# Performance work log

Hardware: AMD Instinct MI355X
Metric: run time of the kernel (lower is better)

## Reference

```python
import jax, jax.numpy as jnp
import numpy as np

B, L, H, N, NL = 2, 160000, 128, 64, 4
TS, MR, CLS, LMAX = 1001, 16, 88, 1024
REP = TS * MR  # 16016


def setup_inputs() -> dict:
    key = jax.random.key(0)
    ks = jax.random.split(key, 16)
    def g(k, shape, s=0.02):
        return jax.random.normal(k, shape, jnp.float32) * s
    return {
        "x": jax.random.normal(ks[0], (B, L), jnp.float32),
        "enc_w": g(ks[1], (1, H), 1.0),
        "enc_b": g(ks[2], (H,)),
        "log_dt": jax.random.uniform(ks[3], (NL, H), jnp.float32, float(np.log(1e-3)), float(np.log(1e-1))),
        "log_A_real": jnp.log(0.5 * jnp.ones((NL, H, N), jnp.float32)),
        "A_imag": jnp.tile((np.pi * np.arange(N, dtype=np.float32))[None, None, :], (NL, H, 1)),
        "C_re": g(ks[4], (NL, H, N), 0.5 ** 0.5),
        "C_im": g(ks[5], (NL, H, N), 0.5 ** 0.5),
        "D": g(ks[6], (NL, H), 1.0),
        "out_w": g(ks[7], (NL, 2 * H, H), H ** -0.5),
        "out_b": g(ks[8], (NL, 2 * H)),
        "ln_g": jnp.ones((NL, H), jnp.float32),
        "ln_b": jnp.zeros((NL, H), jnp.float32),
        "dec_w": g(ks[9], (H, REP), H ** -0.5),
        "dec_b": g(ks[10], (REP,)),
        "head_w": g(ks[11], (4, MR, CLS), MR ** -0.5),
        "head_b": g(ks[12], (4, CLS)),
    }


def _s4_layer(u, log_dt, log_A_real, A_imag, C_re, C_im, D, out_w, out_b):
    # u: (B, H, L). S4D-style diagonal SSM kernel of length LMAX + FFT causal conv.
    dt = jnp.exp(log_dt)                         # (H,)
    A = -jnp.exp(log_A_real) + 1j * A_imag       # (H, N)
    C = C_re + 1j * C_im                         # (H, N)
    dtA = A * dt[:, None]                        # (H, N)
    Ct = C * (jnp.exp(dtA) - 1.0) / A            # ZOH-ish discretization
    l = jnp.arange(LMAX)
    vand = jnp.exp(dtA[:, :, None] * l)          # (H, N, LMAX) Vandermonde
    K = 2.0 * jnp.real(jnp.einsum('hn,hnl->hl', Ct, vand))  # (H, LMAX)
    n = L + LMAX                                 # linear (causal) conv via FFT
    uf = jnp.fft.rfft(u, n=n)                    # (B, H, n//2+1)
    kf = jnp.fft.rfft(K, n=n)                    # (H, n//2+1)
    y = jnp.fft.irfft(uf * kf[None], n=n)[..., :L]
    y = y + D[None, :, None] * u                 # skip connection
    y = jax.nn.gelu(y)
    # position-wise output linear H -> 2H, then GLU
    z = jnp.einsum('bhl,ph->bpl', y, out_w) + out_b[None, :, None]
    a, b = jnp.split(z, 2, axis=1)
    return a * jax.nn.sigmoid(b)


def _layernorm(v, g, b):
    # v: (B, L, H), normalize over H
    mu = v.mean(-1, keepdims=True)
    var = v.var(-1, keepdims=True)
    return (v - mu) / jnp.sqrt(var + 1e-5) * g + b


def reference(x, enc_w, enc_b, log_dt, log_A_real, A_imag, C_re, C_im, D,
              out_w, out_b, ln_g, ln_b, dec_w, dec_b, head_w, head_b):
    # encoder: (B, L, 1) -> (B, L, H)
    h = x[..., None] * enc_w[0][None, None, :] + enc_b  # (B, L, H)
    u = jnp.swapaxes(h, 1, 2)                            # (B, H, L)
    for i in range(NL):
        z = _s4_layer(u, log_dt[i], log_A_real[i], A_imag[i], C_re[i], C_im[i],
                      D[i], out_w[i], out_b[i])
        u = z + u                                        # residual
        v = _layernorm(jnp.swapaxes(u, 1, 2), ln_g[i], ln_b[i])  # post-norm
        u = jnp.swapaxes(v, 1, 2)
    feat = jnp.swapaxes(u, 1, 2).mean(axis=1)            # (B, H) mean-pool over L
    rep = feat @ dec_w + dec_b                           # (B, REP)
    rep = rep.reshape(B, TS, MR)                         # (B, 1001, 16)
    # 4 heads: [reg_onset, reg_offset, frame, velocity] stacked -> (4, B, TS, CLS)
    outs = jnp.einsum('btm,kmc->kbtc', rep, head_w) + head_b[:, None, None, :]
    return outs
```

## Files before the change

kernel.cpp:

```cpp
#include <hip/hip_runtime.h>
#include <math.h>

#define B_ 2
#define L_ 160000
#define H_ 128
#define N_ 64
#define NL_ 4
#define LMAX_ 1024
#define TS_ 1001
#define MR_ 16
#define CLS_ 88
#define REP_ 16016

#define NSUB_ 79
#define NJ_ 40
#define WIN_ 3208
#define WINS_ 3216
#define OUTB_ 2048
#define KE_STRIDE_ 1536

typedef unsigned short ushort_t;
typedef unsigned int uint_t;
typedef short bf16x8 __attribute__((ext_vector_type(8)));
typedef float f32x4 __attribute__((ext_vector_type(4)));

__device__ __forceinline__ float bf2f(ushort_t h) {
  uint_t u = ((uint_t)h) << 16;
  return __uint_as_float(u);
}
__device__ __forceinline__ ushort_t f2bf(float f) {
  uint_t u = __float_as_uint(f);
  uint_t r = (u + 0x7fffu + ((u >> 16) & 1u)) >> 16;
  return (ushort_t)r;
}

__global__ __launch_bounds__(256) void k_encode(const float* __restrict__ x,
                                                const float* __restrict__ enc_w,
                                                const float* __restrict__ enc_b,
                                                ushort_t* __restrict__ u) {
  int idx = blockIdx.x * 256 + threadIdx.x;
  int idx8 = idx * 8;
  int b = idx8 / (H_ * L_);
  int rem = idx8 - b * (H_ * L_);
  int h = rem / L_;
  int l = rem - h * L_;
  float w = enc_w[h], bb = enc_b[h];
  float4 x0 = *(const float4*)(x + b * L_ + l);
  float4 x1 = *(const float4*)(x + b * L_ + l + 4);
  union { ushort_t s[8]; uint4 v; } o;
  o.s[0] = f2bf(x0.x * w + bb); o.s[1] = f2bf(x0.y * w + bb);
  o.s[2] = f2bf(x0.z * w + bb); o.s[3] = f2bf(x0.w * w + bb);
  o.s[4] = f2bf(x1.x * w + bb); o.s[5] = f2bf(x1.y * w + bb);
  o.s[6] = f2bf(x1.z * w + bb); o.s[7] = f2bf(x1.w * w + bb);
  *(uint4*)(u + (size_t)(b * H_ + h) * L_ + l) = o.v;
}

__global__ __launch_bounds__(256) void k_ct(const float* __restrict__ log_dt,
                                            const float* __restrict__ log_A_real,
                                            const float* __restrict__ A_imag,
                                            const float* __restrict__ C_re,
                                            const float* __restrict__ C_im,
                                            float* __restrict__ ct,
                                            float* __restrict__ feat) {
  int idx = blockIdx.x * 256 + threadIdx.x;
  if (idx < B_ * H_) feat[idx] = 0.f;
  if (idx >= NL_ * H_ * N_) return;
  int h = (idx / N_) % H_;
  int i = idx / (N_ * H_);
  float dt = expf(log_dt[i * H_ + h]);
  float are = -expf(log_A_real[idx]);
  float aim = A_imag[idx];
  float dr = are * dt, di = aim * dt;
  float e = expf(dr);
  float si, co;
  sincosf(di, &si, &co);
  float er = e * co - 1.0f;
  float ei = e * si;
  float den = are * are + aim * aim;
  float qr = (er * are + ei * aim) / den;
  float qi = (ei * are - er * aim) / den;
  float cr = C_re[idx], cim = C_im[idx];
  double dd = (double)aim * (double)dt * 0.15915494309189535;
  dd -= floor(dd);
  uint_t P = (uint_t)(unsigned long long)(dd * 4294967296.0);
  ct[idx * 4 + 0] = dr;
  ct[idx * 4 + 1] = __uint_as_float(P);
  ct[idx * 4 + 2] = cr * qr - cim * qi;
  ct[idx * 4 + 3] = cr * qi + cim * qr;
}

__global__ __launch_bounds__(256) void k_ke(const float* __restrict__ ct,
                                            ushort_t* __restrict__ Ke) {
  int q = blockIdx.x & 3;
  int ih = blockIdx.x >> 2;
  __shared__ float4 cs[N_];
  if (threadIdx.x < N_) cs[threadIdx.x] = ((const float4*)ct)[ih * N_ + threadIdx.x];
  __syncthreads();
  for (int s = q * 384 + threadIdx.x; s < (q + 1) * 384; s += 256) {
    int d = s - 256;
    float val = 0.f;
    if (d >= 0 && d < LMAX_) {
      float fl = (float)d;
      float acc = 0.f;
      #pragma unroll 4
      for (int n = 0; n < N_; n++) {
        float4 qv = cs[n];
        float e = __expf(qv.x * fl);
        uint_t ph = __float_as_uint(qv.y) * (uint_t)d;
        float ang = (float)ph * 2.3283064365386963e-10f;
        float si = __builtin_amdgcn_sinf(ang);
        float co = __builtin_amdgcn_cosf(ang);
        acc += e * (qv.z * co - qv.w * si);
      }
      val = 2.f * acc;
    }
    Ke[(size_t)ih * KE_STRIDE_ + s] = f2bf(val);
  }
}

__global__ __launch_bounds__(256) void k_wprep(const float* __restrict__ W,
                                               ushort_t* __restrict__ Wb) {
  int idx = blockIdx.x * 256 + threadIdx.x;
  Wb[idx] = f2bf(W[idx]);
}

__global__ __launch_bounds__(256) void k_conv_mfma(const ushort_t* __restrict__ u,
                                                   const ushort_t* __restrict__ Ke,
                                                   const float* __restrict__ Dv,
                                                   ushort_t* __restrict__ y,
                                                   int layer) {
  int sub = blockIdx.x % NSUB_;
  int bh = blockIdx.x / NSUB_;
  int h = bh & (H_ - 1);
  int O0 = sub * OUTB_;
  int Gmax = O0 + 2063;
  __shared__ ushort_t win[4 * WINS_];
  __shared__ ushort_t kes[KE_STRIDE_];
  int tid = threadIdx.x;
  int lane = tid & 63, w = tid >> 6;
  int m = lane & 15, g = lane >> 4;

  {
    const ushort_t* keh0 = Ke + (size_t)(layer * H_ + h) * KE_STRIDE_;
    if (tid < KE_STRIDE_ / 8)
      *(bf16x8*)(kes + 8 * tid) = *(const bf16x8*)(keh0 + 8 * tid);
  }

  const ushort_t* ubh = u + (size_t)bh * L_;
  for (int T = tid; T < WIN_ / 8; T += 256) {
    int topt = Gmax - 8 * T;
    ushort_t vb[16];
    if (topt - 15 >= 0 && topt < L_) {
      union { uint4 q[2]; ushort_t s[16]; } ld;
      ld.q[0] = *(const uint4*)(ubh + topt - 15);
      ld.q[1] = *(const uint4*)(ubh + topt - 7);
      #pragma unroll
      for (int d = 0; d < 16; d++) vb[d] = ld.s[15 - d];
    } else {
      #pragma unroll
      for (int d = 0; d < 16; d++) {
        int gl = topt - d;
        vb[d] = (gl >= 0 && gl < L_) ? ubh[gl] : (ushort_t)0;
      }
    }
    #pragma unroll
    for (int p = 0; p < 4; p++) {
      union { bf16x8 v; ushort_t s[8]; } gr;
      #pragma unroll
      for (int e = 0; e < 8; e++) gr.s[e] = vb[p + e];
      *(bf16x8*)((char*)win + p * (2 * WINS_) + 16 * T) = gr.v;
    }
  }
  __syncthreads();

  const char* wb = (const char*)win;
  const ushort_t* kf0 = kes + 16 * m + 8 * g;
  int l0A = O0 + (w << 9);
  f32x4 accA = {0.f, 0.f, 0.f, 0.f}, accB = {0.f, 0.f, 0.f, 0.f};
  int t0 = Gmax - l0A - m + 8 * g - 256;
  bf16x8 ring[8];
  #pragma unroll
  for (int s = -8; s < NJ_; s++) {
    int tS = t0 + (s << 5);
    int pS = tS & 3;
    const char* base = wb + pS * (2 * WINS_) + 2 * (tS - pS);
    union { bf16x8 v; short4 h[2]; } f;
    f.h[0] = *(const short4*)base;
    f.h[1] = *(const short4*)(base + 8);
    if (s >= 0)
      accA = __builtin_amdgcn_mfma_f32_16x16x32_bf16(f.v, ring[s & 7], accA, 0, 0, 0);
    if (s <= 31) {
      bf16x8 kn = *(const bf16x8*)(kf0 + 32 * (s + 8));
      accB = __builtin_amdgcn_mfma_f32_16x16x32_bf16(f.v, kn, accB, 0, 0, 0);
      ring[(s + 8) & 7] = kn;
    }
  }

  float Dh = Dv[layer * H_ + h];
  ushort_t* ybh = y + (size_t)bh * L_;
  #pragma unroll
  for (int tile = 0; tile < 2; tile++) {
    f32x4 acc = tile ? accB : accA;
    int l0 = l0A + tile * 256;
    int outb = l0 + 16 * m + 4 * g;
    int tu = Gmax - outb - 3;
    int pu = tu & 3;
    union { short4 s4; ushort_t us[4]; } uu;
    uu.s4 = *(const short4*)(wb + pu * (2 * WINS_) + 2 * (tu - pu));
    union { ushort_t s[4]; short4 v; } pk;
    #pragma unroll
    for (int r = 0; r < 4; r++) {
      float uval = bf2f(uu.us[3 - r]);
      float v = acc[r] + Dh * uval;
      float z2 = 1.5957691216057308f * (v + 0.044715f * v * v * v);
      pk.s[r] = f2bf(v / (1.f + __expf(-z2)));
    }
    if (outb < L_) *(short4*)(ybh + outb) = pk.v;
  }
}

__global__ __launch_bounds__(256) void k_fused(const ushort_t* __restrict__ y,
                                               const ushort_t* __restrict__ Wb,
                                               const float* __restrict__ ob,
                                               ushort_t* __restrict__ u,
                                               const float* __restrict__ lng,
                                               const float* __restrict__ lnb,
                                               int last,
                                               float* __restrict__ feat) {
  __shared__ ushort_t yT[64 * 136];
  __shared__ float redS[4 * 64] __attribute__((aligned(16)));
  __shared__ float redQ[4 * 64] __attribute__((aligned(16)));
  __shared__ float redM[64] __attribute__((aligned(16)));
  __shared__ float redR[64] __attribute__((aligned(16)));
  int lblk = blockIdx.x, b = blockIdx.y;
  int lc0 = lblk * 64;
  int tid = threadIdx.x;
  int lane = tid & 63, w = tid >> 6;
  int m = lane & 15, g = lane >> 4;

  bf16x8 Wf[4][4];
  #pragma unroll
  for (int pj = 0; pj < 4; pj++) {
    int pbase = (pj < 2) ? (32 * w + 16 * pj) : (128 + 32 * w + 16 * (pj - 2));
    const ushort_t* wrow = Wb + (pbase + m) * 128 + 8 * g;
    #pragma unroll
    for (int ks = 0; ks < 4; ks++)
      Wf[pj][ks] = *(const bf16x8*)(wrow + 32 * ks);
  }

  short4 uoh[2][4];
  float oba[2], obs[2], gam[2], bet[2];
  #pragma unroll
  for (int pj = 0; pj < 2; pj++) {
    int pa = 32 * w + 16 * pj + m;
    const ushort_t* urow = u + (size_t)(b * H_ + pa) * L_ + lc0;
    #pragma unroll
    for (int lj = 0; lj < 4; lj++)
      uoh[pj][lj] = *(const short4*)(urow + 16 * lj + 4 * g);
    oba[pj] = ob[pa];
    obs[pj] = ob[pa + 128];
    gam[pj] = lng[pa];
    bet[pj] = lnb[pa];
  }

  {
    int s = tid & 7;
    int kkb = tid >> 3;
    #pragma unroll
    for (int p = 0; p < 4; p++) {
      int kk = kkb + 32 * p;
      const ushort_t* yp = y + ((size_t)b * H_ + kk) * L_ + lc0 + 8 * s;
      uint4 vv = *(const uint4*)yp;
      const ushort_t* hp = (const ushort_t*)&vv;
      int sw = 8 * ((kk >> 3) ^ s) + (kk & 7);
      #pragma unroll
      for (int e = 0; e < 8; e++)
        yT[(8 * s + e) * 136 + sw] = hp[e];
    }
  }
  __syncthreads();

  f32x4 acc[4][4];
  #pragma unroll
  for (int pj = 0; pj < 4; pj++)
    #pragma unroll
    for (int lj = 0; lj < 4; lj++) acc[pj][lj] = (f32x4){0.f, 0.f, 0.f, 0.f};
  #pragma unroll
  for (int ks = 0; ks < 4; ks++) {
    bf16x8 yf[4];
    #pragma unroll
    for (int lj = 0; lj < 4; lj++) {
      int l = 16 * lj + m;
      yf[lj] = *(const bf16x8*)(yT + l * 136 + 8 * ((4 * ks + g) ^ (l >> 3)));
    }
    #pragma unroll
    for (int pj = 0; pj < 4; pj++)
      #pragma unroll
      for (int lj = 0; lj < 4; lj++)
        acc[pj][lj] = __builtin_amdgcn_mfma_f32_16x16x32_bf16(yf[lj], Wf[pj][ks],
                                                              acc[pj][lj], 0, 0, 0);
  }

  #pragma unroll
  for (int pj = 0; pj < 2; pj++) {
    #pragma unroll
    for (int lj = 0; lj < 4; lj++) {
      #pragma unroll
      for (int r = 0; r < 4; r++) {
        float a = acc[pj][lj][r] + oba[pj];
        float sv = acc[pj + 2][lj][r] + obs[pj];
        float uor = bf2f(((const ushort_t*)&uoh[pj][lj])[r]);
        acc[pj][lj][r] = a * (1.f / (1.f + __expf(-sv))) + uor;
      }
    }
  }

  #pragma unroll
  for (int lj = 0; lj < 4; lj++) {
    #pragma unroll
    for (int r = 0; r < 4; r++) {
      float v0 = acc[0][lj][r], v1 = acc[1][lj][r];
      float s = v0 + v1, q = v0 * v0 + v1 * v1;
      s += __shfl_xor(s, 1);  q += __shfl_xor(q, 1);
      s += __shfl_xor(s, 2);  q += __shfl_xor(q, 2);
      s += __shfl_xor(s, 4);  q += __shfl_xor(q, 4);
      s += __shfl_xor(s, 8);  q += __shfl_xor(q, 8);
      if (m == 0) {
        int l = 16 * lj + 4 * g + r;
        redS[w * 64 + l] = s;
        redQ[w * 64 + l] = q;
      }
    }
  }
  __syncthreads();
  if (tid < 64) {
    float s = redS[tid] + redS[64 + tid] + redS[128 + tid] + redS[192 + tid];
    float q = redQ[tid] + redQ[64 + tid] + redQ[128 + tid] + redQ[192 + tid];
    float mean = s * (1.f / 128.f);
    float var = q * (1.f / 128.f) - mean * mean;
    redM[tid] = mean;
    redR[tid] = rsqrtf(var + 1e-5f);
  }
  __syncthreads();

  #pragma unroll
  for (int pj = 0; pj < 2; pj++) {
    int pa = 32 * w + 16 * pj + m;
    ushort_t* urow = u + (size_t)(b * H_ + pa) * L_ + lc0;
    float pool = 0.f;
    #pragma unroll
    for (int lj = 0; lj < 4; lj++) {
      int l0 = 16 * lj + 4 * g;
      f32x4 mn = *(const f32x4*)(redM + l0);
      f32x4 rs = *(const f32x4*)(redR + l0);
      if (!last) {
        union { ushort_t s[4]; short4 v; } pk;
        #pragma unroll
        for (int r = 0; r < 4; r++)
          pk.s[r] = f2bf((acc[pj][lj][r] - mn[r]) * rs[r] * gam[pj] + bet[pj]);
        *(short4*)(urow + l0) = pk.v;
      } else {
        #pragma unroll
        for (int r = 0; r < 4; r++)
          pool += (acc[pj][lj][r] - mn[r]) * rs[r] * gam[pj] + bet[pj];
      }
    }
    if (last) {
      pool += __shfl_xor(pool, 16);
      pool += __shfl_xor(pool, 32);
      if (g == 0) atomicAdd(&feat[b * H_ + pa], pool * (1.f / L_));
    }
  }
}

__global__ __launch_bounds__(256) void k_dec(const float* __restrict__ feat,
                                             const float* __restrict__ dw,
                                             const float* __restrict__ db,
                                             float* __restrict__ rep) {
  int idx = blockIdx.x * 256 + threadIdx.x;
  if (idx >= B_ * REP_) return;
  int b = idx / REP_, r = idx - b * REP_;
  float s = db[r];
  #pragma unroll 8
  for (int h = 0; h < H_; h++) s = fmaf(feat[b * H_ + h], dw[h * REP_ + r], s);
  rep[idx] = s;
}

__global__ __launch_bounds__(256) void k_head(const float* __restrict__ rep,
                                              const float* __restrict__ hw,
                                              const float* __restrict__ hb,
                                              float* __restrict__ out) {
  int idx = blockIdx.x * 256 + threadIdx.x;
  if (idx >= 4 * B_ * TS_ * CLS_) return;
  int c = idx % CLS_;
  int t = (idx / CLS_) % TS_;
  int b = (idx / (CLS_ * TS_)) % B_;
  int k = idx / (CLS_ * TS_ * B_);
  float s = hb[k * CLS_ + c];
  const float* rp = rep + ((long long)b * TS_ + t) * MR_;
  #pragma unroll
  for (int m = 0; m < MR_; m++) s = fmaf(rp[m], hw[(k * MR_ + m) * CLS_ + c], s);
  out[idx] = s;
}

extern "C" void kernel_launch(void* const* d_in, const int* in_sizes, int n_in,
                              void* d_out, int out_size, void* d_ws, size_t ws_size,
                              hipStream_t stream) {
  const float* x = (const float*)d_in[0];
  const float* enc_w = (const float*)d_in[1];
  const float* enc_b = (const float*)d_in[2];
  const float* log_dt = (const float*)d_in[3];
  const float* log_A_real = (const float*)d_in[4];
  const float* A_imag = (const float*)d_in[5];
  const float* C_re = (const float*)d_in[6];
  const float* C_im = (const float*)d_in[7];
  const float* Dv = (const float*)d_in[8];
  const float* out_w = (const float*)d_in[9];
  const float* out_b = (const float*)d_in[10];
  const float* ln_g = (const float*)d_in[11];
  const float* ln_b = (const float*)d_in[12];
  const float* dec_w = (const float*)d_in[13];
  const float* dec_b = (const float*)d_in[14];
  const float* head_w = (const float*)d_in[15];
  const float* head_b = (const float*)d_in[16];

  if (ws_size < 167000000ULL) return;

  float* ws = (float*)d_ws;
  ushort_t* u = (ushort_t*)ws;
  ushort_t* y = (ushort_t*)(ws + 20480000);
  ushort_t* Ke = (ushort_t*)(ws + 20480000 + 20480000);
  float* ct = ws + 20480000 + 20480000 + 393216;
  ushort_t* Wb = (ushort_t*)(ct + 131072);
  float* feat = ct + 131072 + 65536;
  float* rep = feat + 256;

  k_encode<<<(B_ * H_ * L_ / 8 + 255) / 256, 256, 0, stream>>>(x, enc_w, enc_b, u);
  k_ct<<<(NL_ * H_ * N_ + 255) / 256, 256, 0, stream>>>(log_dt, log_A_real, A_imag,
                                                        C_re, C_im, ct, feat);
  k_ke<<<NL_ * H_ * 4, 256, 0, stream>>>(ct, Ke);
  k_wprep<<<NL_ * 256 * 128 / 256, 256, 0, stream>>>(out_w, Wb);

  for (int i = 0; i < NL_; i++) {
    k_conv_mfma<<<B_ * H_ * NSUB_, 256, 0, stream>>>(u, Ke, Dv, y, i);
    k_fused<<<dim3(L_ / 64, B_), 256, 0, stream>>>(
        y, Wb + (size_t)i * 256 * 128, out_b + i * 256, u,
        ln_g + i * H_, ln_b + i * H_, (i == NL_ - 1) ? 1 : 0, feat);
  }
  k_dec<<<(B_ * REP_ + 255) / 256, 256, 0, stream>>>(feat, dec_w, dec_b, rep);
  k_head<<<(4 * B_ * TS_ * CLS_ + 255) / 256, 256, 0, stream>>>(rep, head_w, head_b,
                                                               (float*)d_out);
}
```

Before: 929.7 us.

## Process four L-tiles per block in k_fused with register prefetch of next tile

The fused projection/GLU/LayerNorm kernel now walks four consecutive 64-column tiles per block instead of one. The weight fragments and per-channel constants are loaded once and reused across the four tiles. The next tile's y and residual u values are prefetched into registers while the current tile's MFMAs and reductions run. The grid shrinks by a factor of four. In exchange, register pressure rises from the extra prefetch buffers, which may lower occupancy, and there are fewer blocks to spread across the CUs.

```diff
diff --git a/kernel.cpp b/kernel.cpp
--- a/kernel.cpp
+++ b/kernel.cpp
@@ -233,10 +233,11 @@
   __shared__ float redM[64] __attribute__((aligned(16)));
   __shared__ float redR[64] __attribute__((aligned(16)));
   int lblk = blockIdx.x, b = blockIdx.y;
-  int lc0 = lblk * 64;
   int tid = threadIdx.x;
   int lane = tid & 63, w = tid >> 6;
   int m = lane & 15, g = lane >> 4;
+  int s = tid & 7, kkb = tid >> 3;
+  int Lbase = lblk * 256;
 
   bf16x8 Wf[4][4];
   #pragma unroll
@@ -247,125 +248,163 @@
     for (int ks = 0; ks < 4; ks++)
       Wf[pj][ks] = *(const bf16x8*)(wrow + 32 * ks);
   }
-
-  short4 uoh[2][4];
   float oba[2], obs[2], gam[2], bet[2];
   #pragma unroll
   for (int pj = 0; pj < 2; pj++) {
     int pa = 32 * w + 16 * pj + m;
-    const ushort_t* urow = u + (size_t)(b * H_ + pa) * L_ + lc0;
-    #pragma unroll
-    for (int lj = 0; lj < 4; lj++)
-      uoh[pj][lj] = *(const short4*)(urow + 16 * lj + 4 * g);
     oba[pj] = ob[pa];
     obs[pj] = ob[pa + 128];
     gam[pj] = lng[pa];
     bet[pj] = lnb[pa];
   }
 
-  {
-    int s = tid & 7;
-    int kkb = tid >> 3;
+  uint4 sr[4];
+  short4 un[2][4];
+  #pragma unroll
+  for (int p = 0; p < 4; p++)
+    sr[p] = *(const uint4*)(y + ((size_t)b * H_ + kkb + 32 * p) * L_ + Lbase + 8 * s);
+  #pragma unroll
+  for (int pj = 0; pj < 2; pj++) {
+    int pa = 32 * w + 16 * pj + m;
+    const ushort_t* urow = u + (size_t)(b * H_ + pa) * L_ + Lbase;
+    #pragma unroll
+    for (int lj = 0; lj < 4; lj++)
+      un[pj][lj] = *(const short4*)(urow + 16 * lj + 4 * g);
+  }
+
+  float poolAcc[2] = {0.f, 0.f};
+
+  #pragma unroll
+  for (int st = 0; st < 4; st++) {
+    int lc0 = Lbase + st * 64;
+
     #pragma unroll
     for (int p = 0; p < 4; p++) {
       int kk = kkb + 32 * p;
-      const ushort_t* yp = y + ((size_t)b * H_ + kk) * L_ + lc0 + 8 * s;
-      uint4 vv = *(const uint4*)yp;
-      const ushort_t* hp = (const ushort_t*)&vv;
+      const ushort_t* hp = (const ushort_t*)&sr[p];
       int sw = 8 * ((kk >> 3) ^ s) + (kk & 7);
       #pragma unroll
       for (int e = 0; e < 8; e++)
         yT[(8 * s + e) * 136 + sw] = hp[e];
     }
-  }
-  __syncthreads();
-
-  f32x4 acc[4][4];
-  #pragma unroll
-  for (int pj = 0; pj < 4; pj++)
-    #pragma unroll
-    for (int lj = 0; lj < 4; lj++) acc[pj][lj] = (f32x4){0.f, 0.f, 0.f, 0.f};
-  #pragma unroll
-  for (int ks = 0; ks < 4; ks++) {
-    bf16x8 yf[4];
+    __syncthreads();
+
+    uint4 srn[4];
+    short4 unn[2][4];
+    if (st < 3) {
+      int lc1 = lc0 + 64;
+      #pragma unroll
+      for (int p = 0; p < 4; p++)
+        srn[p] = *(const uint4*)(y + ((size_t)b * H_ + kkb + 32 * p) * L_ + lc1 + 8 * s);
+      #pragma unroll
+      for (int pj = 0; pj < 2; pj++) {
+        int pa = 32 * w + 16 * pj + m;
+        const ushort_t* urow = u + (size_t)(b * H_ + pa) * L_ + lc1;
+        #pragma unroll
+        for (int lj = 0; lj < 4; lj++)
+          unn[pj][lj] = *(const short4*)(urow + 16 * lj + 4 * g);
+      }
+    }
+
+    f32x4 acc[4][4];
+    #pragma unroll
+    for (int pj = 0; pj < 4; pj++)
+      #pragma unroll
+      for (int lj = 0; lj < 4; lj++) acc[pj][lj] = (f32x4){0.f, 0.f, 0.f, 0.f};
+    #pragma unroll
+    for (int ks = 0; ks < 4; ks++) {
+      bf16x8 yf[4];
+      #pragma unroll
+      for (int lj = 0; lj < 4; lj++) {
+        int l = 16 * lj + m;
+        yf[lj] = *(const bf16x8*)(yT + l * 136 + 8 * ((4 * ks + g) ^ (l >> 3)));
+      }
+      #pragma unroll
+      for (int pj = 0; pj < 4; pj++)
+        #pragma unroll
+        for (int lj = 0; lj < 4; lj++)
+          acc[pj][lj] = __builtin_amdgcn_mfma_f32_16x16x32_bf16(yf[lj], Wf[pj][ks],
+                                                                acc[pj][lj], 0, 0, 0);
+    }
+
+    #pragma unroll
+    for (int pj = 0; pj < 2; pj++) {
+      #pragma unroll
+      for (int lj = 0; lj < 4; lj++) {
+        #pragma unroll
+        for (int r = 0; r < 4; r++) {
+          float a = acc[pj][lj][r] + oba[pj];
+          float sv = acc[pj + 2][lj][r] + obs[pj];
+          float uor = bf2f(((const ushort_t*)&un[pj][lj])[r]);
+          acc[pj][lj][r] = a * (1.f / (1.f + __expf(-sv))) + uor;
+        }
+      }
+    }
+
     #pragma unroll
     for (int lj = 0; lj < 4; lj++) {
-      int l = 16 * lj + m;
-      yf[lj] = *(const bf16x8*)(yT + l * 136 + 8 * ((4 * ks + g) ^ (l >> 3)));
-    }
-    #pragma unroll
-    for (int pj = 0; pj < 4; pj++)
-      #pragma unroll
-      for (int lj = 0; lj < 4; lj++)
-        acc[pj][lj] = __builtin_amdgcn_mfma_f32_16x16x32_bf16(yf[lj], Wf[pj][ks],
-                                                              acc[pj][lj], 0, 0, 0);
-  }
-
-  #pragma unroll
-  for (int pj = 0; pj < 2; pj++) {
-    #pragma unroll
-    for (int lj = 0; lj < 4; lj++) {
       #pragma unroll
       for (int r = 0; r < 4; r++) {
-        float a = acc[pj][lj][r] + oba[pj];
-        float sv = acc[pj + 2][lj][r] + obs[pj];
-        float uor = bf2f(((const ushort_t*)&uoh[pj][lj])[r]);
-        acc[pj][lj][r] = a * (1.f / (1.f + __expf(-sv))) + uor;
-      }
-    }
-  }
-
-  #pragma unroll
-  for (int lj = 0; lj < 4; lj++) {
-    #pragma unroll
-    for (int r = 0; r < 4; r++) {
-      float v0 = acc[0][lj][r], v1 = acc[1][lj][r];
-      float s = v0 + v1, q = v0 * v0 + v1 * v1;
-      s += __shfl_xor(s, 1);  q += __shfl_xor(q, 1);
-      s += __shfl_xor(s, 2);  q += __shfl_xor(q, 2);
-      s += __shfl_xor(s, 4);  q += __shfl_xor(q, 4);
-      s += __shfl_xor(s, 8);  q += __shfl_xor(q, 8);
-      if (m == 0) {
-        int l = 16 * lj + 4 * g + r;
-        redS[w * 64 + l] = s;
-        redQ[w * 64 + l] = q;
-      }
-    }
-  }
-  __syncthreads();
-  if (tid < 64) {
-    float s = redS[tid] + redS[64 + tid] + redS[128 + tid] + redS[192 + tid];
-    float q = redQ[tid] + redQ[64 + tid] + redQ[128 + tid] + redQ[192 + tid];
-    float mean = s * (1.f / 128.f);
-    float var = q * (1.f / 128.f) - mean * mean;
-    redM[tid] = mean;
-    redR[tid] = rsqrtf(var + 1e-5f);
-  }
-  __syncthreads();
-
-  #pragma unroll
-  for (int pj = 0; pj < 2; pj++) {
-    int pa = 32 * w + 16 * pj + m;
-    ushort_t* urow = u + (size_t)(b * H_ + pa) * L_ + lc0;
-    float pool = 0.f;
-    #pragma unroll
-    for (int lj = 0; lj < 4; lj++) {
-      int l0 = 16 * lj + 4 * g;
-      f32x4 mn = *(const f32x4*)(redM + l0);
-      f32x4 rs = *(const f32x4*)(redR + l0);
-      if (!last) {
-        union { ushort_t s[4]; short4 v; } pk;
-        #pragma unroll
-        for (int r = 0; r < 4; r++)
-          pk.s[r] = f2bf((acc[pj][lj][r] - mn[r]) * rs[r] * gam[pj] + bet[pj]);
-        *(short4*)(urow + l0) = pk.v;
-      } else {
-        #pragma unroll
-        for (int r = 0; r < 4; r++)
-          pool += (acc[pj][lj][r] - mn[r]) * rs[r] * gam[pj] + bet[pj];
-      }
-    }
-    if (last) {
+        float v0 = acc[0][lj][r], v1 = acc[1][lj][r];
+        float sm = v0 + v1, q = v0 * v0 + v1 * v1;
+        sm += __shfl_xor(sm, 1);  q += __shfl_xor(q, 1);
+        sm += __shfl_xor(sm, 2);  q += __shfl_xor(q, 2);
+        sm += __shfl_xor(sm, 4);  q += __shfl_xor(q, 4);
+        sm += __shfl_xor(sm, 8);  q += __shfl_xor(q, 8);
+        if (m == 0) {
+          int l = 16 * lj + 4 * g + r;
+          redS[w * 64 + l] = sm;
+          redQ[w * 64 + l] = q;
+        }
+      }
+    }
+    __syncthreads();
+    if (tid < 64) {
+      float sm = redS[tid] + redS[64 + tid] + redS[128 + tid] + redS[192 + tid];
+      float q = redQ[tid] + redQ[64 + tid] + redQ[128 + tid] + redQ[192 + tid];
+      float mean = sm * (1.f / 128.f);
+      float var = q * (1.f / 128.f) - mean * mean;
+      redM[tid] = mean;
+      redR[tid] = rsqrtf(var + 1e-5f);
+    }
+    __syncthreads();
+
+    #pragma unroll
+    for (int pj = 0; pj < 2; pj++) {
+      int pa = 32 * w + 16 * pj + m;
+      ushort_t* urow = u + (size_t)(b * H_ + pa) * L_ + lc0;
+      #pragma unroll
+      for (int lj = 0; lj < 4; lj++) {
+        int l0 = 16 * lj + 4 * g;
+        f32x4 mn = *(const f32x4*)(redM + l0);
+        f32x4 rs = *(const f32x4*)(redR + l0);
+        if (!last) {
+          union { ushort_t sx[4]; short4 v; } pk;
+          #pragma unroll
+          for (int r = 0; r < 4; r++)
+            pk.sx[r] = f2bf((acc[pj][lj][r] - mn[r]) * rs[r] * gam[pj] + bet[pj]);
+          *(short4*)(urow + l0) = pk.v;
+        } else {
+          #pragma unroll
+          for (int r = 0; r < 4; r++)
+            poolAcc[pj] += (acc[pj][lj][r] - mn[r]) * rs[r] * gam[pj] + bet[pj];
+        }
+      }
+    }
+
+    #pragma unroll
+    for (int p = 0; p < 4; p++) sr[p] = srn[p];
+    #pragma unroll
+    for (int pj = 0; pj < 2; pj++)
+      #pragma unroll
+      for (int lj = 0; lj < 4; lj++) un[pj][lj] = unn[pj][lj];
+  }
+
+  if (last) {
+    #pragma unroll
+    for (int pj = 0; pj < 2; pj++) {
+      int pa = 32 * w + 16 * pj + m;
+      float pool = poolAcc[pj];
       pool += __shfl_xor(pool, 16);
       pool += __shfl_xor(pool, 32);
       if (g == 0) atomicAdd(&feat[b * H_ + pa], pool * (1.f / L_));
@@ -443,7 +482,7 @@
 
   for (int i = 0; i < NL_; i++) {
     k_conv_mfma<<<B_ * H_ * NSUB_, 256, 0, stream>>>(u, Ke, Dv, y, i);
-    k_fused<<<dim3(L_ / 64, B_), 256, 0, stream>>>(
+    k_fused<<<dim3(L_ / 256, B_), 256, 0, stream>>>(
         y, Wb + (size_t)i * 256 * 128, out_b + i * 256, u,
         ln_g + i * H_, ln_b + i * H_, (i == NL_ - 1) ? 1 : 0, feat);
   }
```

Measured after the change: 1.011 ms. 1.09x slower.
